# Kernel optimization log

Measured on AMD Instinct MI355X. Metric: run time of the kernel, lower is better.

Reference implementation:

```python
import jax, jax.numpy as jnp
import numpy as np

D_MODEL = 1024
NHEAD = 16
HEAD_DIM = D_MODEL // NHEAD
B, S = 4, 2048


def setup_inputs() -> dict:
    key = jax.random.key(0)
    ks = jax.random.split(key, 10)
    scale = 1.0 / np.sqrt(D_MODEL)
    inp = {
        "x": jax.random.normal(ks[0], (B, S, D_MODEL), dtype=jnp.float32),
        "y": jax.random.normal(ks[1], (B, S, D_MODEL), dtype=jnp.float32),
        "wq": jax.random.normal(ks[2], (D_MODEL, D_MODEL), dtype=jnp.float32) * scale,
        "bq": jnp.zeros((D_MODEL,), dtype=jnp.float32),
        "wk": jax.random.normal(ks[3], (D_MODEL, D_MODEL), dtype=jnp.float32) * scale,
        "bk": jnp.zeros((D_MODEL,), dtype=jnp.float32),
        "wv": jax.random.normal(ks[4], (D_MODEL, D_MODEL), dtype=jnp.float32) * scale,
        "bv": jnp.zeros((D_MODEL,), dtype=jnp.float32),
        "wo": jax.random.normal(ks[5], (D_MODEL, D_MODEL), dtype=jnp.float32) * scale,
        "bo": jnp.zeros((D_MODEL,), dtype=jnp.float32),
    }
    return inp


def reference(x, y, wq, bq, wk, bk, wv, bv, wo, bo):
    # Linear projections (torch nn.Linear: x @ W.T + b; here weights stored as [in, out])
    q = x @ wq + bq  # [B, S, D]
    k = y @ wk + bk
    v = y @ wv + bv
    # split heads -> [B, H, S, Dh]
    def heads(t):
        return t.reshape(B, S, NHEAD, HEAD_DIM).transpose(0, 2, 1, 3)
    q, k, v = heads(q), heads(k), heads(v)
    scores = jnp.einsum("bhqd,bhkd->bhqk", q, k) / jnp.sqrt(jnp.float32(HEAD_DIM))
    attn = jax.nn.softmax(scores, axis=-1)  # dropout = identity in eval mode
    out = jnp.einsum("bhqk,bhkd->bhqd", attn, v)
    out = out.transpose(0, 2, 1, 3).reshape(B, S, D_MODEL)
    return out @ wo + bo
```

## Files before the change

kernel.cpp:

```cpp
#include <hip/hip_runtime.h>
#include <stdint.h>

#define D_MODEL 1024
#define NHEAD 16
#define HEAD_DIM 64
#define BATCH 4
#define SEQ 2048
#define ROWS (BATCH*SEQ)

typedef __attribute__((ext_vector_type(8))) short short8;
typedef __attribute__((ext_vector_type(4))) float f32x4;
typedef __attribute__((ext_vector_type(2))) unsigned int u32x2;
typedef unsigned short u16;
typedef unsigned int u32;

#define QSCALE 0.18033688011112042f

__device__ __forceinline__ u16 f2b(float f) {
  union { float f; uint32_t u; } in; in.f = f;
  uint32_t u = in.u;
  return (u16)((u + 0x7FFFu + ((u >> 16) & 1u)) >> 16);
}

__device__ __forceinline__ void async_lds16(const void* g, void* l) {
  __builtin_amdgcn_global_load_lds(
      (const __attribute__((address_space(1))) uint32_t*)g,
      (__attribute__((address_space(3))) uint32_t*)l,
      16, 0, 0);
}

__device__ __forceinline__ u32 pack_bf16(float lo, float hi) {
  union { float f; uint32_t u; } a, b; a.f = lo; b.f = hi;
  return __builtin_amdgcn_perm(b.u + 0x8000u, a.u + 0x8000u, 0x07060302u);
}

__global__ void __launch_bounds__(256) pre_kernel(const float* __restrict__ x,
                                                  const float* __restrict__ y,
                                                  const float* __restrict__ wq,
                                                  const float* __restrict__ wk,
                                                  const float* __restrict__ wv,
                                                  const float* __restrict__ wo,
                                                  u16* __restrict__ xb,
                                                  u16* __restrict__ yb,
                                                  u16* __restrict__ wtbase) {
  __shared__ u16 tile[64 * 65];
  int gid = blockIdx.x;
  if (gid < 16384) {
    const float* in = (gid >= 8192) ? y : x;
    u16* out = (gid >= 8192) ? yb : xb;
    int i = (gid & 8191) * 256 + threadIdx.x;
    float4 v = ((const float4*)in)[i];
    ushort4 o;
    o.x = f2b(v.x); o.y = f2b(v.y); o.z = f2b(v.z); o.w = f2b(v.w);
    ((ushort4*)out)[i] = o;
  } else {
    int idx = gid - 16384;
    int z = idx >> 8;
    int rem = idx & 255;
    const float* w = (z == 0) ? wq : (z == 1 ? wk : (z == 2 ? wv : wo));
    u16* wt = wtbase + (size_t)z * D_MODEL * D_MODEL;
    int t = threadIdx.x;
    int c = t & 63, rb = t >> 6;
    int k0 = (rem & 15) * 64, n0 = (rem >> 4) * 64;
#pragma unroll
    for (int i = 0; i < 16; ++i) {
      int r = rb + i * 4;
      tile[c * 65 + r] = f2b(w[(size_t)(k0 + r) * D_MODEL + n0 + c]);
    }
    __syncthreads();
#pragma unroll
    for (int i = 0; i < 16; ++i) {
      int r = rb + i * 4;
      wt[(size_t)(n0 + r) * D_MODEL + k0 + c] = tile[r * 65 + c];
    }
  }
}

template <int MODE>
__device__ __forceinline__ void gemm_bt_core(const u16* __restrict__ A,
                                             const u16* __restrict__ Bt,
                                             const float* __restrict__ bias,
                                             void* __restrict__ Cout, float scale,
                                             int m0, int n0,
                                             u16 (* __restrict__ As)[128 * 32],
                                             u16 (* __restrict__ Bs)[128 * 32]) {
  constexpr int K = 1024, N = 1024;
  constexpr bool SWAP = (MODE != 2);
  int tid = threadIdx.x;
  int wave = tid >> 6, lane = tid & 63;
  int quad = lane >> 4, l16 = lane & 15;
  int wm = wave & 1, wn = wave >> 1;

  f32x4 acc[4][4];
#pragma unroll
  for (int p = 0; p < 4; ++p)
#pragma unroll
    for (int q = 0; q < 4; ++q) acc[p][q] = f32x4{0.f, 0.f, 0.f, 0.f};

  int srow = lane >> 2;
  int scol = (lane & 3) * 16;

  for (int k0 = 0; k0 < K; k0 += 64) {
#pragma unroll
    for (int kh = 0; kh < 2; ++kh) {
#pragma unroll
      for (int i = 0; i < 2; ++i) {
        int c = wave * 2 + i;
        const char* ga = (const char*)(A + (size_t)(m0 + c * 16 + srow) * K + k0 + kh * 32) + scol;
        async_lds16(ga, (char*)As[kh] + c * 1024);
        const char* gb = (const char*)(Bt + (size_t)(n0 + c * 16 + srow) * K + k0 + kh * 32) + scol;
        async_lds16(gb, (char*)Bs[kh] + c * 1024);
      }
    }
    __syncthreads();

#pragma unroll
    for (int kh = 0; kh < 2; ++kh) {
      short8 fa[4], fb[4];
#pragma unroll
      for (int p = 0; p < 4; ++p)
        fa[p] = SWAP
          ? *(const short8*)(Bs[kh] + (wn * 64 + p * 16 + l16) * 32 + quad * 8)
          : *(const short8*)(As[kh] + (wm * 64 + p * 16 + l16) * 32 + quad * 8);
#pragma unroll
      for (int q = 0; q < 4; ++q)
        fb[q] = SWAP
          ? *(const short8*)(As[kh] + (wm * 64 + q * 16 + l16) * 32 + quad * 8)
          : *(const short8*)(Bs[kh] + (wn * 64 + q * 16 + l16) * 32 + quad * 8);
#pragma unroll
      for (int p = 0; p < 4; ++p)
#pragma unroll
        for (int q = 0; q < 4; ++q)
          acc[p][q] = __builtin_amdgcn_mfma_f32_16x16x32_bf16(fa[p], fb[q], acc[p][q], 0, 0, 0);
    }
    __syncthreads();
  }

  if (MODE == 2) {
    int sblk = n0 + wn * 64;
    int bb = sblk >> 11;
    int ssb = sblk & 2047;
#pragma unroll
    for (int p = 0; p < 4; ++p) {
      int dbase = m0 + wm * 64 + p * 16 + quad * 4;
      float4 b4 = *(const float4*)(bias + dbase);
#pragma unroll
      for (int r = 0; r < 4; ++r) {
        int d = dbase + r;
        float bv = ((const float*)&b4)[r];
        u32 lo = pack_bf16(acc[p][0][r] + bv, acc[p][1][r] + bv);
        u32 hi = pack_bf16(acc[p][2][r] + bv, acc[p][3][r] + bv);
        size_t vtrow = ((size_t)bb * 16 + (d >> 6)) * 64 + (d & 63);
        *(u32x2*)((u16*)Cout + vtrow * 2048 + ssb + 4 * l16) = u32x2{lo, hi};
      }
    }
  } else {
#pragma unroll
    for (int p = 0; p < 4; ++p) {
      int nbase = n0 + wn * 64 + p * 16 + quad * 4;
      float4 b4 = *(const float4*)(bias + nbase);
#pragma unroll
      for (int q = 0; q < 4; ++q) {
        size_t mrow = (size_t)(m0 + wm * 64 + q * 16 + l16);
        float v0 = (acc[p][q][0] + b4.x) * scale;
        float v1 = (acc[p][q][1] + b4.y) * scale;
        float v2 = (acc[p][q][2] + b4.z) * scale;
        float v3 = (acc[p][q][3] + b4.w) * scale;
        if (MODE == 1) {
          *(f32x4*)((float*)Cout + mrow * N + nbase) = f32x4{v0, v1, v2, v3};
        } else {
          *(u32x2*)((u16*)Cout + mrow * N + nbase) = u32x2{pack_bf16(v0, v1), pack_bf16(v2, v3)};
        }
      }
    }
  }
}

__global__ void __launch_bounds__(256, 4) gemm_qkv_kernel(
    const u16* __restrict__ xb, const u16* __restrict__ yb,
    const u16* __restrict__ wqT, const u16* __restrict__ wkT, const u16* __restrict__ wvT,
    const float* __restrict__ bq, const float* __restrict__ bk, const float* __restrict__ bv,
    u16* __restrict__ q, u16* __restrict__ k, u16* __restrict__ vt) {
  __shared__ u16 As[2][128 * 32];
  __shared__ u16 Bs[2][128 * 32];
  int bx = blockIdx.x, z = blockIdx.y;
  int xcd = bx & 7, i = bx >> 3;
  int stripe = (xcd * 8 + (i >> 3)) * 128;
  int other  = (i & 7) * 128;
  if (z == 0) {
    gemm_bt_core<0>(xb, wqT, bq, q, QSCALE, stripe, other, As, Bs);
  } else if (z == 1) {
    gemm_bt_core<0>(yb, wkT, bk, k, 1.0f, stripe, other, As, Bs);
  } else {
    gemm_bt_core<2>(wvT, yb, bv, vt, 1.0f, other, stripe, As, Bs);
  }
}

__global__ void __launch_bounds__(256, 4) gemm_o_kernel(const u16* __restrict__ ao,
                                                        const u16* __restrict__ woT,
                                                        const float* __restrict__ bo,
                                                        float* __restrict__ out) {
  __shared__ u16 As[2][128 * 32];
  __shared__ u16 Bs[2][128 * 32];
  int bx = blockIdx.x, by = blockIdx.y;
  int m0 = (bx * 8 + (by >> 3)) * 128;
  int n0 = (by & 7) * 128;
  gemm_bt_core<1>(ao, woT, bo, out, 1.0f, m0, n0, As, Bs);
}

__global__ void __launch_bounds__(256, 4) attn_kernel(const u16* __restrict__ Q,
                                                      const u16* __restrict__ Kp,
                                                      const u16* __restrict__ Vt,
                                                      u16* __restrict__ Outp) {
  __shared__ u16 Ks[2][64 * 64];
  __shared__ u16 Vts[2][64 * 64];
  __shared__ u16 Ps[4][16 * 64];

  int tid = threadIdx.x, wave = tid >> 6, lane = tid & 63;
  int quad = lane >> 4, l16 = lane & 15;
  int bh = blockIdx.x;
  int b = bh >> 4, h = bh & 15;
  int q0 = blockIdx.y * 128 + wave * 32;
  size_t gbase = (size_t)b * SEQ * D_MODEL;
  const u16* kbase = Kp + gbase + (size_t)h * HEAD_DIM;
  const u16* vbase = Vt + (size_t)bh * HEAD_DIM * SEQ;
  const u16* qrow = Q + gbase + (size_t)q0 * D_MODEL + (size_t)h * HEAD_DIM;

  short8 aq[2][2];
#pragma unroll
  for (int rs = 0; rs < 2; ++rs)
#pragma unroll
    for (int dc = 0; dc < 2; ++dc)
      aq[rs][dc] = *(const short8*)(qrow + (size_t)(rs * 16 + l16) * D_MODEL + dc * 32 + quad * 8);

  const short8 onesb = short8{0x3F80, 0x3F80, 0x3F80, 0x3F80,
                              0x3F80, 0x3F80, 0x3F80, 0x3F80};

  f32x4 Oacc[2][4];
  f32x4 Lacc[2];
#pragma unroll
  for (int rs = 0; rs < 2; ++rs) {
#pragma unroll
    for (int ni = 0; ni < 4; ++ni) Oacc[rs][ni] = f32x4{0.f, 0.f, 0.f, 0.f};
    Lacc[rs] = f32x4{0.f, 0.f, 0.f, 0.f};
  }

  int c0 = tid, c1 = 256 + tid;
  int krow0 = c0 >> 3, kgp0 = c0 & 7;
  int krow1 = c1 >> 3, kgp1 = c1 & 7;
  size_t koff0 = (size_t)krow0 * D_MODEL + (size_t)((kgp0 ^ (krow0 & 7)) * 8);
  size_t koff1 = (size_t)krow1 * D_MODEL + (size_t)((kgp1 ^ (krow1 & 7)) * 8);
  size_t voff0 = (size_t)krow0 * SEQ + (size_t)((kgp0 ^ (krow0 & 7)) * 8);
  size_t voff1 = (size_t)krow1 * SEQ + (size_t)((kgp1 ^ (krow1 & 7)) * 8);
  int dst0 = wave * 1024;
  int dst1 = 4096 + wave * 1024;

  async_lds16(kbase + koff0, (char*)Ks[0] + dst0);
  async_lds16(kbase + koff1, (char*)Ks[0] + dst1);
  async_lds16(vbase + voff0, (char*)Vts[0] + dst0);
  async_lds16(vbase + voff1, (char*)Vts[0] + dst1);
  const u16* kp0 = kbase + (size_t)64 * D_MODEL + koff0;
  const u16* kp1 = kbase + (size_t)64 * D_MODEL + koff1;
  const u16* vp0 = vbase + 64 + voff0;
  const u16* vp1 = vbase + 64 + voff1;

  constexpr int NT = SEQ / 64;
  for (int t = 0; t < NT; ++t) {
    int cur = t & 1;
    __syncthreads();
    if (t + 1 < NT) {
      async_lds16(kp0, (char*)Ks[cur ^ 1] + dst0);
      async_lds16(kp1, (char*)Ks[cur ^ 1] + dst1);
      async_lds16(vp0, (char*)Vts[cur ^ 1] + dst0);
      async_lds16(vp1, (char*)Vts[cur ^ 1] + dst1);
      kp0 += (size_t)64 * D_MODEL;
      kp1 += (size_t)64 * D_MODEL;
      vp0 += 64;
      vp1 += 64;
    }

    const u16* Kc = Ks[cur];
    const u16* Vc = Vts[cur];
    u16* Pw = Ps[wave];
    int x = l16 & 7;

    short8 kf[4][2];
#pragma unroll
    for (int sub = 0; sub < 4; ++sub) {
      const u16* kr = Kc + (sub * 16 + l16) * 64;
      kf[sub][0] = *(const short8*)(kr + ((quad ^ x) << 3));
      kf[sub][1] = *(const short8*)(kr + (((4 + quad) ^ x) << 3));
    }

    short8 pa[2][2];
#pragma unroll
    for (int rs = 0; rs < 2; ++rs) {
      f32x4 S[4];
      __builtin_amdgcn_s_setprio(1);
#pragma unroll
      for (int sub = 0; sub < 4; ++sub) {
        f32x4 s = f32x4{0.f, 0.f, 0.f, 0.f};
        s = __builtin_amdgcn_mfma_f32_16x16x32_bf16(aq[rs][0], kf[sub][0], s, 0, 0, 0);
        s = __builtin_amdgcn_mfma_f32_16x16x32_bf16(aq[rs][1], kf[sub][1], s, 0, 0, 0);
        S[sub] = s;
      }
      __builtin_amdgcn_s_setprio(0);
#pragma unroll
      for (int r = 0; r < 4; ++r) {
        float p0 = __builtin_amdgcn_exp2f(S[0][r]);
        float p1 = __builtin_amdgcn_exp2f(S[1][r]);
        float p2 = __builtin_amdgcn_exp2f(S[2][r]);
        float p3 = __builtin_amdgcn_exp2f(S[3][r]);
        u32 lo = pack_bf16(p0, p1);
        u32 hi = pack_bf16(p2, p3);
        int row = quad * 4 + r;
        int off = row * 64 + (((l16 >> 1) ^ (row & 7)) << 3) + ((l16 & 1) << 2);
        *(u32x2*)(Pw + off) = u32x2{lo, hi};
      }
#pragma unroll
      for (int kc = 0; kc < 2; ++kc)
        pa[rs][kc] = *(const short8*)(Pw + l16 * 64 + ((((kc << 2) + quad) ^ x) << 3));
    }

    __builtin_amdgcn_s_setprio(1);
#pragma unroll
    for (int kc = 0; kc < 2; ++kc) {
      Lacc[0] = __builtin_amdgcn_mfma_f32_16x16x32_bf16(pa[0][kc], onesb, Lacc[0], 0, 0, 0);
      Lacc[1] = __builtin_amdgcn_mfma_f32_16x16x32_bf16(pa[1][kc], onesb, Lacc[1], 0, 0, 0);
#pragma unroll
      for (int ni = 0; ni < 4; ++ni) {
        int d = ni * 16 + l16;
        short8 bv = *(const short8*)(Vc + d * 64 + ((((kc << 2) + quad) ^ (l16 & 7)) << 3));
        Oacc[0][ni] = __builtin_amdgcn_mfma_f32_16x16x32_bf16(pa[0][kc], bv, Oacc[0][ni], 0, 0, 0);
        Oacc[1][ni] = __builtin_amdgcn_mfma_f32_16x16x32_bf16(pa[1][kc], bv, Oacc[1][ni], 0, 0, 0);
      }
    }
    __builtin_amdgcn_s_setprio(0);
  }

#pragma unroll
  for (int rs = 0; rs < 2; ++rs)
#pragma unroll
    for (int r = 0; r < 4; ++r) {
      float inv = 1.0f / Lacc[rs][r];
      size_t orow = gbase + (size_t)(q0 + rs * 16 + quad * 4 + r) * D_MODEL + (size_t)h * HEAD_DIM;
#pragma unroll
      for (int ni = 0; ni < 4; ++ni)
        Outp[orow + ni * 16 + l16] = f2b(Oacc[rs][ni][r] * inv);
    }
}

extern "C" void kernel_launch(void* const* d_in, const int* in_sizes, int n_in,
                              void* d_out, int out_size, void* d_ws, size_t ws_size,
                              hipStream_t stream) {
  const float* x  = (const float*)d_in[0];
  const float* y  = (const float*)d_in[1];
  const float* wq = (const float*)d_in[2];
  const float* bq = (const float*)d_in[3];
  const float* wk = (const float*)d_in[4];
  const float* bk = (const float*)d_in[5];
  const float* wv = (const float*)d_in[6];
  const float* bv = (const float*)d_in[7];
  const float* wo = (const float*)d_in[8];
  const float* bo = (const float*)d_in[9];
  float* out = (float*)d_out;

  char* ws = (char*)d_ws;
  const size_t SZ_ACT = (size_t)ROWS * D_MODEL * 2;
  const size_t SZ_W   = (size_t)D_MODEL * D_MODEL * 2;
  u16* xb  = (u16*)(ws);
  u16* yb  = (u16*)(ws + SZ_ACT);
  u16* wT  = (u16*)(ws + 2 * SZ_ACT);
  u16* wqT = wT;
  u16* wkT = (u16*)(ws + 2 * SZ_ACT + SZ_W);
  u16* wvT = (u16*)(ws + 2 * SZ_ACT + 2 * SZ_W);
  u16* woT = (u16*)(ws + 2 * SZ_ACT + 3 * SZ_W);
  u16* qb  = (u16*)(ws + 2 * SZ_ACT + 4 * SZ_W);
  u16* kb  = (u16*)(ws + 3 * SZ_ACT + 4 * SZ_W);
  u16* vt  = (u16*)(ws + 4 * SZ_ACT + 4 * SZ_W);
  u16* ao  = (u16*)(ws + 5 * SZ_ACT + 4 * SZ_W);

  pre_kernel<<<dim3(17408), 256, 0, stream>>>(x, y, wq, wk, wv, wo, xb, yb, wT);
  gemm_qkv_kernel<<<dim3(512, 3), 256, 0, stream>>>(xb, yb, wqT, wkT, wvT, bq, bk, bv, qb, kb, vt);
  attn_kernel<<<dim3(64, 16), 256, 0, stream>>>(qb, kb, vt, ao);
  gemm_o_kernel<<<dim3(8, 64), 256, 0, stream>>>(ao, woT, bo, out);
}
```

Measured before the change: 298.8 us.

## Fuse attention and output projection into one kernel with a global barrier

Attention and the output projection GEMM now run in a single persistent-style launch. All 1024 blocks finish their attention tile, synchronize on a device-scope atomic counter, and then the first 512 blocks compute the output GEMM, reusing a shared LDS buffer. This removes one kernel launch and its tail gap. The cost is a spin barrier that only works if all 1024 blocks are co-resident (256 CUs x 4 blocks), idle blocks during the GEMM phase, and an extra memset.

```diff
diff --git a/kernel.cpp b/kernel.cpp
--- a/kernel.cpp
+++ b/kernel.cpp
@@ -196,158 +196,168 @@
   }
 }
 
-__global__ void __launch_bounds__(256, 4) gemm_o_kernel(const u16* __restrict__ ao,
-                                                        const u16* __restrict__ woT,
-                                                        const float* __restrict__ bo,
-                                                        float* __restrict__ out) {
-  __shared__ u16 As[2][128 * 32];
-  __shared__ u16 Bs[2][128 * 32];
-  int bx = blockIdx.x, by = blockIdx.y;
-  int m0 = (bx * 8 + (by >> 3)) * 128;
-  int n0 = (by & 7) * 128;
-  gemm_bt_core<1>(ao, woT, bo, out, 1.0f, m0, n0, As, Bs);
-}
-
-__global__ void __launch_bounds__(256, 4) attn_kernel(const u16* __restrict__ Q,
-                                                      const u16* __restrict__ Kp,
-                                                      const u16* __restrict__ Vt,
-                                                      u16* __restrict__ Outp) {
-  __shared__ u16 Ks[2][64 * 64];
-  __shared__ u16 Vts[2][64 * 64];
-  __shared__ u16 Ps[4][16 * 64];
-
+__global__ void __launch_bounds__(256, 4) attn_o_kernel(
+    const u16* __restrict__ Q, const u16* __restrict__ Kp,
+    const u16* __restrict__ Vt, u16* __restrict__ ao,
+    const u16* __restrict__ woT, const float* __restrict__ bo,
+    float* __restrict__ out, u32* __restrict__ bar) {
+  __shared__ u16 smem[20480];
+  int g = blockIdx.x;
   int tid = threadIdx.x, wave = tid >> 6, lane = tid & 63;
   int quad = lane >> 4, l16 = lane & 15;
-  int bh = blockIdx.x;
-  int b = bh >> 4, h = bh & 15;
-  int q0 = blockIdx.y * 128 + wave * 32;
-  size_t gbase = (size_t)b * SEQ * D_MODEL;
-  const u16* kbase = Kp + gbase + (size_t)h * HEAD_DIM;
-  const u16* vbase = Vt + (size_t)bh * HEAD_DIM * SEQ;
-  const u16* qrow = Q + gbase + (size_t)q0 * D_MODEL + (size_t)h * HEAD_DIM;
-
-  short8 aq[2][2];
-#pragma unroll
-  for (int rs = 0; rs < 2; ++rs)
-#pragma unroll
-    for (int dc = 0; dc < 2; ++dc)
-      aq[rs][dc] = *(const short8*)(qrow + (size_t)(rs * 16 + l16) * D_MODEL + dc * 32 + quad * 8);
-
-  const short8 onesb = short8{0x3F80, 0x3F80, 0x3F80, 0x3F80,
-                              0x3F80, 0x3F80, 0x3F80, 0x3F80};
-
-  f32x4 Oacc[2][4];
-  f32x4 Lacc[2];
-#pragma unroll
-  for (int rs = 0; rs < 2; ++rs) {
-#pragma unroll
-    for (int ni = 0; ni < 4; ++ni) Oacc[rs][ni] = f32x4{0.f, 0.f, 0.f, 0.f};
-    Lacc[rs] = f32x4{0.f, 0.f, 0.f, 0.f};
-  }
-
-  int c0 = tid, c1 = 256 + tid;
-  int krow0 = c0 >> 3, kgp0 = c0 & 7;
-  int krow1 = c1 >> 3, kgp1 = c1 & 7;
-  size_t koff0 = (size_t)krow0 * D_MODEL + (size_t)((kgp0 ^ (krow0 & 7)) * 8);
-  size_t koff1 = (size_t)krow1 * D_MODEL + (size_t)((kgp1 ^ (krow1 & 7)) * 8);
-  size_t voff0 = (size_t)krow0 * SEQ + (size_t)((kgp0 ^ (krow0 & 7)) * 8);
-  size_t voff1 = (size_t)krow1 * SEQ + (size_t)((kgp1 ^ (krow1 & 7)) * 8);
-  int dst0 = wave * 1024;
-  int dst1 = 4096 + wave * 1024;
-
-  async_lds16(kbase + koff0, (char*)Ks[0] + dst0);
-  async_lds16(kbase + koff1, (char*)Ks[0] + dst1);
-  async_lds16(vbase + voff0, (char*)Vts[0] + dst0);
-  async_lds16(vbase + voff1, (char*)Vts[0] + dst1);
-  const u16* kp0 = kbase + (size_t)64 * D_MODEL + koff0;
-  const u16* kp1 = kbase + (size_t)64 * D_MODEL + koff1;
-  const u16* vp0 = vbase + 64 + voff0;
-  const u16* vp1 = vbase + 64 + voff1;
-
-  constexpr int NT = SEQ / 64;
-  for (int t = 0; t < NT; ++t) {
-    int cur = t & 1;
-    __syncthreads();
-    if (t + 1 < NT) {
-      async_lds16(kp0, (char*)Ks[cur ^ 1] + dst0);
-      async_lds16(kp1, (char*)Ks[cur ^ 1] + dst1);
-      async_lds16(vp0, (char*)Vts[cur ^ 1] + dst0);
-      async_lds16(vp1, (char*)Vts[cur ^ 1] + dst1);
-      kp0 += (size_t)64 * D_MODEL;
-      kp1 += (size_t)64 * D_MODEL;
-      vp0 += 64;
-      vp1 += 64;
-    }
-
-    const u16* Kc = Ks[cur];
-    const u16* Vc = Vts[cur];
-    u16* Pw = Ps[wave];
-    int x = l16 & 7;
-
-    short8 kf[4][2];
-#pragma unroll
-    for (int sub = 0; sub < 4; ++sub) {
-      const u16* kr = Kc + (sub * 16 + l16) * 64;
-      kf[sub][0] = *(const short8*)(kr + ((quad ^ x) << 3));
-      kf[sub][1] = *(const short8*)(kr + (((4 + quad) ^ x) << 3));
-    }
-
-    short8 pa[2][2];
+
+  {
+    char* KsB = (char*)smem;
+    char* VtsB = (char*)smem + 16384;
+    u16* Pw = smem + 16384 / 2 + 8192 + wave * 1024;
+    Pw = smem + 16384 + wave * 1024;
+
+    int bh = g & 63;
+    int b = bh >> 4, h = bh & 15;
+    int q0 = (g >> 6) * 128 + wave * 32;
+    size_t gbase = (size_t)b * SEQ * D_MODEL;
+    const u16* kbase = Kp + gbase + (size_t)h * HEAD_DIM;
+    const u16* vbase = Vt + (size_t)bh * HEAD_DIM * SEQ;
+    const u16* qrow = Q + gbase + (size_t)q0 * D_MODEL + (size_t)h * HEAD_DIM;
+
+    short8 aq[2][2];
+#pragma unroll
+    for (int rs = 0; rs < 2; ++rs)
+#pragma unroll
+      for (int dc = 0; dc < 2; ++dc)
+        aq[rs][dc] = *(const short8*)(qrow + (size_t)(rs * 16 + l16) * D_MODEL + dc * 32 + quad * 8);
+
+    const short8 onesb = short8{0x3F80, 0x3F80, 0x3F80, 0x3F80,
+                                0x3F80, 0x3F80, 0x3F80, 0x3F80};
+
+    f32x4 Oacc[2][4];
+    f32x4 Lacc[2];
 #pragma unroll
     for (int rs = 0; rs < 2; ++rs) {
-      f32x4 S[4];
+#pragma unroll
+      for (int ni = 0; ni < 4; ++ni) Oacc[rs][ni] = f32x4{0.f, 0.f, 0.f, 0.f};
+      Lacc[rs] = f32x4{0.f, 0.f, 0.f, 0.f};
+    }
+
+    int c0 = tid, c1 = 256 + tid;
+    int krow0 = c0 >> 3, kgp0 = c0 & 7;
+    int krow1 = c1 >> 3, kgp1 = c1 & 7;
+    size_t koff0 = (size_t)krow0 * D_MODEL + (size_t)((kgp0 ^ (krow0 & 7)) * 8);
+    size_t koff1 = (size_t)krow1 * D_MODEL + (size_t)((kgp1 ^ (krow1 & 7)) * 8);
+    size_t voff0 = (size_t)krow0 * SEQ + (size_t)((kgp0 ^ (krow0 & 7)) * 8);
+    size_t voff1 = (size_t)krow1 * SEQ + (size_t)((kgp1 ^ (krow1 & 7)) * 8);
+    int dst0 = wave * 1024;
+    int dst1 = 4096 + wave * 1024;
+
+    async_lds16(kbase + koff0, KsB + dst0);
+    async_lds16(kbase + koff1, KsB + dst1);
+    async_lds16(vbase + voff0, VtsB + dst0);
+    async_lds16(vbase + voff1, VtsB + dst1);
+    const u16* kp0 = kbase + (size_t)64 * D_MODEL + koff0;
+    const u16* kp1 = kbase + (size_t)64 * D_MODEL + koff1;
+    const u16* vp0 = vbase + 64 + voff0;
+    const u16* vp1 = vbase + 64 + voff1;
+
+    constexpr int NT = SEQ / 64;
+    for (int t = 0; t < NT; ++t) {
+      int cur = t & 1;
+      __syncthreads();
+      if (t + 1 < NT) {
+        async_lds16(kp0, KsB + (cur ^ 1) * 8192 + dst0);
+        async_lds16(kp1, KsB + (cur ^ 1) * 8192 + dst1);
+        async_lds16(vp0, VtsB + (cur ^ 1) * 8192 + dst0);
+        async_lds16(vp1, VtsB + (cur ^ 1) * 8192 + dst1);
+        kp0 += (size_t)64 * D_MODEL;
+        kp1 += (size_t)64 * D_MODEL;
+        vp0 += 64;
+        vp1 += 64;
+      }
+
+      const u16* Kc = (const u16*)(KsB + cur * 8192);
+      const u16* Vc = (const u16*)(VtsB + cur * 8192);
+      int x = l16 & 7;
+
+      short8 kf[4][2];
+#pragma unroll
+      for (int sub = 0; sub < 4; ++sub) {
+        const u16* kr = Kc + (sub * 16 + l16) * 64;
+        kf[sub][0] = *(const short8*)(kr + ((quad ^ x) << 3));
+        kf[sub][1] = *(const short8*)(kr + (((4 + quad) ^ x) << 3));
+      }
+
+      short8 pa[2][2];
+#pragma unroll
+      for (int rs = 0; rs < 2; ++rs) {
+        f32x4 S[4];
+        __builtin_amdgcn_s_setprio(1);
+#pragma unroll
+        for (int sub = 0; sub < 4; ++sub) {
+          f32x4 s = f32x4{0.f, 0.f, 0.f, 0.f};
+          s = __builtin_amdgcn_mfma_f32_16x16x32_bf16(aq[rs][0], kf[sub][0], s, 0, 0, 0);
+          s = __builtin_amdgcn_mfma_f32_16x16x32_bf16(aq[rs][1], kf[sub][1], s, 0, 0, 0);
+          S[sub] = s;
+        }
+        __builtin_amdgcn_s_setprio(0);
+#pragma unroll
+        for (int r = 0; r < 4; ++r) {
+          float p0 = __builtin_amdgcn_exp2f(S[0][r]);
+          float p1 = __builtin_amdgcn_exp2f(S[1][r]);
+          float p2 = __builtin_amdgcn_exp2f(S[2][r]);
+          float p3 = __builtin_amdgcn_exp2f(S[3][r]);
+          u32 lo = pack_bf16(p0, p1);
+          u32 hi = pack_bf16(p2, p3);
+          int row = quad * 4 + r;
+          int off = row * 64 + (((l16 >> 1) ^ (row & 7)) << 3) + ((l16 & 1) << 2);
+          *(u32x2*)(Pw + off) = u32x2{lo, hi};
+        }
+#pragma unroll
+        for (int kc = 0; kc < 2; ++kc)
+          pa[rs][kc] = *(const short8*)(Pw + l16 * 64 + ((((kc << 2) + quad) ^ x) << 3));
+      }
+
       __builtin_amdgcn_s_setprio(1);
 #pragma unroll
-      for (int sub = 0; sub < 4; ++sub) {
-        f32x4 s = f32x4{0.f, 0.f, 0.f, 0.f};
-        s = __builtin_amdgcn_mfma_f32_16x16x32_bf16(aq[rs][0], kf[sub][0], s, 0, 0, 0);
-        s = __builtin_amdgcn_mfma_f32_16x16x32_bf16(aq[rs][1], kf[sub][1], s, 0, 0, 0);
-        S[sub] = s;
+      for (int kc = 0; kc < 2; ++kc) {
+        Lacc[0] = __builtin_amdgcn_mfma_f32_16x16x32_bf16(pa[0][kc], onesb, Lacc[0], 0, 0, 0);
+        Lacc[1] = __builtin_amdgcn_mfma_f32_16x16x32_bf16(pa[1][kc], onesb, Lacc[1], 0, 0, 0);
+#pragma unroll
+        for (int ni = 0; ni < 4; ++ni) {
+          int d = ni * 16 + l16;
+          short8 bv = *(const short8*)(Vc + d * 64 + ((((kc << 2) + quad) ^ (l16 & 7)) << 3));
+          Oacc[0][ni] = __builtin_amdgcn_mfma_f32_16x16x32_bf16(pa[0][kc], bv, Oacc[0][ni], 0, 0, 0);
+          Oacc[1][ni] = __builtin_amdgcn_mfma_f32_16x16x32_bf16(pa[1][kc], bv, Oacc[1][ni], 0, 0, 0);
+        }
       }
       __builtin_amdgcn_s_setprio(0);
+    }
+
+#pragma unroll
+    for (int rs = 0; rs < 2; ++rs)
 #pragma unroll
       for (int r = 0; r < 4; ++r) {
-        float p0 = __builtin_amdgcn_exp2f(S[0][r]);
-        float p1 = __builtin_amdgcn_exp2f(S[1][r]);
-        float p2 = __builtin_amdgcn_exp2f(S[2][r]);
-        float p3 = __builtin_amdgcn_exp2f(S[3][r]);
-        u32 lo = pack_bf16(p0, p1);
-        u32 hi = pack_bf16(p2, p3);
-        int row = quad * 4 + r;
-        int off = row * 64 + (((l16 >> 1) ^ (row & 7)) << 3) + ((l16 & 1) << 2);
-        *(u32x2*)(Pw + off) = u32x2{lo, hi};
-      }
-#pragma unroll
-      for (int kc = 0; kc < 2; ++kc)
-        pa[rs][kc] = *(const short8*)(Pw + l16 * 64 + ((((kc << 2) + quad) ^ x) << 3));
-    }
-
-    __builtin_amdgcn_s_setprio(1);
-#pragma unroll
-    for (int kc = 0; kc < 2; ++kc) {
-      Lacc[0] = __builtin_amdgcn_mfma_f32_16x16x32_bf16(pa[0][kc], onesb, Lacc[0], 0, 0, 0);
-      Lacc[1] = __builtin_amdgcn_mfma_f32_16x16x32_bf16(pa[1][kc], onesb, Lacc[1], 0, 0, 0);
-#pragma unroll
-      for (int ni = 0; ni < 4; ++ni) {
-        int d = ni * 16 + l16;
-        short8 bv = *(const short8*)(Vc + d * 64 + ((((kc << 2) + quad) ^ (l16 & 7)) << 3));
-        Oacc[0][ni] = __builtin_amdgcn_mfma_f32_16x16x32_bf16(pa[0][kc], bv, Oacc[0][ni], 0, 0, 0);
-        Oacc[1][ni] = __builtin_amdgcn_mfma_f32_16x16x32_bf16(pa[1][kc], bv, Oacc[1][ni], 0, 0, 0);
-      }
-    }
-    __builtin_amdgcn_s_setprio(0);
-  }
-
-#pragma unroll
-  for (int rs = 0; rs < 2; ++rs)
-#pragma unroll
-    for (int r = 0; r < 4; ++r) {
-      float inv = 1.0f / Lacc[rs][r];
-      size_t orow = gbase + (size_t)(q0 + rs * 16 + quad * 4 + r) * D_MODEL + (size_t)h * HEAD_DIM;
-#pragma unroll
-      for (int ni = 0; ni < 4; ++ni)
-        Outp[orow + ni * 16 + l16] = f2b(Oacc[rs][ni][r] * inv);
-    }
+        float inv = 1.0f / Lacc[rs][r];
+        size_t orow = gbase + (size_t)(q0 + rs * 16 + quad * 4 + r) * D_MODEL + (size_t)h * HEAD_DIM;
+#pragma unroll
+        for (int ni = 0; ni < 4; ++ni)
+          ao[orow + ni * 16 + l16] = f2b(Oacc[rs][ni][r] * inv);
+      }
+  }
+
+  __syncthreads();
+  if (tid == 0) {
+    __hip_atomic_fetch_add(bar, 1u, __ATOMIC_ACQ_REL, __HIP_MEMORY_SCOPE_AGENT);
+    while (__hip_atomic_load(bar, __ATOMIC_ACQUIRE, __HIP_MEMORY_SCOPE_AGENT) < 1024u)
+      __builtin_amdgcn_s_sleep(8);
+  }
+  __syncthreads();
+
+  if (g < 512) {
+    int bx = g & 7, by = g >> 3;
+    int m0 = (bx * 8 + (by >> 3)) * 128;
+    int n0 = (by & 7) * 128;
+    gemm_bt_core<1>(ao, woT, bo, out, 1.0f, m0, n0,
+                    (u16(*)[128 * 32])smem, (u16(*)[128 * 32])(smem + 8192));
+  }
 }
 
 extern "C" void kernel_launch(void* const* d_in, const int* in_sizes, int n_in,
@@ -379,9 +389,10 @@
   u16* kb  = (u16*)(ws + 3 * SZ_ACT + 4 * SZ_W);
   u16* vt  = (u16*)(ws + 4 * SZ_ACT + 4 * SZ_W);
   u16* ao  = (u16*)(ws + 5 * SZ_ACT + 4 * SZ_W);
-
+  u32* bar = (u32*)(ws + 6 * SZ_ACT + 4 * SZ_W);
+
+  hipMemsetAsync(bar, 0, 4, stream);
   pre_kernel<<<dim3(17408), 256, 0, stream>>>(x, y, wq, wk, wv, wo, xb, yb, wT);
   gemm_qkv_kernel<<<dim3(512, 3), 256, 0, stream>>>(xb, yb, wqT, wkT, wvT, bq, bk, bv, qb, kb, vt);
-  attn_kernel<<<dim3(64, 16), 256, 0, stream>>>(qb, kb, vt, ao);
-  gemm_o_kernel<<<dim3(8, 64), 256, 0, stream>>>(ao, woT, bo, out);
-}
+  attn_o_kernel<<<dim3(1024), 256, 0, stream>>>(qb, kb, vt, ao, woT, bo, out, bar);
+}
```

Measured after the change: 543.4 us. +81.8%, slower.
